# Kernel optimization log

Hardware: AMD Instinct MI355X
Metric: run time of the kernel (lower is better)

The kernel has to match this reference:

```python
import jax, jax.numpy as jnp
import numpy as np

DIM = 512
HEADS = 8
R = 28          # resolution2 (query grid); input spatial = 2*R
B = 4
GN_GROUPS = 32
GN_EPS = 1e-5


def _conv(x, w, stride=1, pad=0, groups=1):
    return jax.lax.conv_general_dilated(
        x, w, (stride, stride), [(pad, pad), (pad, pad)],
        dimension_numbers=('NCHW', 'OIHW', 'NCHW'), feature_group_count=groups)


def _gn(x, w, b, groups=GN_GROUPS, eps=GN_EPS):
    Bn, C, H, W = x.shape
    xg = x.reshape(Bn, groups, C // groups, H, W)
    m = xg.mean(axis=(2, 3, 4), keepdims=True)
    v = xg.var(axis=(2, 3, 4), keepdims=True)
    xg = (xg - m) * jax.lax.rsqrt(v + eps)
    return xg.reshape(Bn, C, H, W) * w[None, :, None, None] + b[None, :, None, None]


def _l2norm_axis1(x, eps=1e-12):
    # torch F.normalize default: dim=1 (here: the heads axis), clamp_min on norm
    n = jnp.sqrt(jnp.sum(x * x, axis=1, keepdims=True))
    return x / jnp.maximum(n, eps)


def _hardswish(x):
    return x * jnp.clip(x + 3.0, 0.0, 6.0) * (1.0 / 6.0)


def _bias_idxs(r):
    # offset (|2*i1-i2|, |2*j1-j2|) -> unique id oy*(2r)+ox; table [r*r, (2r)*(2r)]
    oy = np.abs(2 * np.arange(r)[:, None] - np.arange(2 * r)[None, :])  # [r, 2r]
    ox = oy
    idx = oy[:, None, :, None] * (2 * r) + ox[None, :, None, :]  # [r, r, 2r, 2r]
    return jnp.asarray(idx.reshape(r * r, 4 * r * r), dtype=jnp.int32)


def setup_inputs() -> dict:
    key = jax.random.key(0)
    ks = jax.random.split(key, 16)
    dim, heads, r = DIM, HEADS, R
    cin = dim // 2
    H = 2 * r
    rn = lambda k, s, sc: jax.random.normal(k, s, jnp.float32) * sc
    ones = lambda s: jnp.ones(s, jnp.float32)
    zeros = lambda s: jnp.zeros(s, jnp.float32)
    return {
        'x': rn(ks[0], (B, cin, H, H), 1.0),
        'q_local_w': rn(ks[1], (cin, 1, 3, 3), 0.1),
        'q_local_b': zeros((cin,)),
        'q_proj_w': rn(ks[2], (dim, cin, 1, 1), 0.05),
        'q_proj_b': zeros((dim,)),
        'q_gn_w': ones((dim,)), 'q_gn_b': zeros((dim,)),
        'k_w': rn(ks[3], (dim, cin, 1, 1), 0.05),
        'k_gn_w': ones((dim,)), 'k_gn_b': zeros((dim,)),
        'v_w': rn(ks[4], (dim, cin, 1, 1), 0.05),
        'v_gn_w': ones((dim,)), 'v_gn_b': zeros((dim,)),
        'loc_w': rn(ks[5], (dim, dim // heads, 3, 3), 0.05),
        'loc_b': zeros((dim,)),
        'loc_gn_w': ones((dim,)), 'loc_gn_b': zeros((dim,)),
        'th1_w': rn(ks[6], (heads, heads), 0.3),
        'th2_w': rn(ks[7], (heads, heads), 0.3),
        'out_w': rn(ks[8], (dim, dim, 1, 1), 0.05),
        'out_gn_w': ones((dim,)), 'out_gn_b': zeros((dim,)),
        'proj_w': rn(ks[9], (dim, cin, 3, 3), 0.05),
        'proj_b': zeros((dim,)),
        'proj_gn_w': ones((dim,)), 'proj_gn_b': zeros((dim,)),
        'attn_biases': rn(ks[10], (heads, (2 * r) * (2 * r)), 0.02),
        'bias_idxs': _bias_idxs(r),
    }


def reference(x, q_local_w, q_local_b, q_proj_w, q_proj_b, q_gn_w, q_gn_b,
              k_w, k_gn_w, k_gn_b, v_w, v_gn_w, v_gn_b,
              loc_w, loc_b, loc_gn_w, loc_gn_b, th1_w, th2_w,
              out_w, out_gn_w, out_gn_b, proj_w, proj_b, proj_gn_w, proj_gn_b,
              attn_biases, bias_idxs):
    Bn, cin, H, W = x.shape
    dim, heads = DIM, HEADS
    hd = dim // heads
    N = H * W
    r = H // 2
    N2 = r * r
    scale = hd ** -0.5

    # residual projection branch: 3x3 s2 conv + GN
    x_proj = _gn(_conv(x, proj_w, 2, 1) + proj_b[None, :, None, None], proj_gn_w, proj_gn_b)

    # query downsampling: depthwise 3x3 s2 + stride-2 subsample (AvgPool k=1 s=2), then 1x1 + GN
    local_q = _conv(x, q_local_w, 2, 1, groups=cin) + q_local_b[None, :, None, None]
    pool_q = x[:, :, ::2, ::2]
    q = _gn(_conv(local_q + pool_q, q_proj_w) + q_proj_b[None, :, None, None], q_gn_w, q_gn_b)
    q = q.reshape(Bn, heads, hd, N2).transpose(0, 1, 3, 2)          # [B,h,N2,hd]

    k = _gn(_conv(x, k_w), k_gn_w, k_gn_b).reshape(Bn, heads, hd, N)  # [B,h,hd,N]

    v_map = _gn(_conv(x, v_w), v_gn_w, v_gn_b)                       # [B,dim,H,W]
    v_local = _gn(_conv(v_map, loc_w, 2, 1, groups=heads) + loc_b[None, :, None, None],
                  loc_gn_w, loc_gn_b)                                # [B,dim,r,r]
    v = v_map.reshape(Bn, heads, hd, N).transpose(0, 1, 3, 2)        # [B,h,N,hd]

    # cosine attention (normalized over heads axis, faithful to F.normalize dim=1)
    qn = _l2norm_axis1(q)
    kn = _l2norm_axis1(k)
    attn = jnp.einsum('bhqd,bhdn->bhqn', qn, kn) * scale \
        + attn_biases[:, bias_idxs][None]                            # [B,h,N2,N]

    # talking heads: 1x1 conv over heads axis, pre- and post-softmax
    attn = jnp.einsum('oi,biqn->boqn', th1_w, attn)
    attn = jax.nn.softmax(attn, axis=-1)
    attn = jnp.einsum('oi,biqn->boqn', th2_w, attn)

    out = jnp.einsum('bhqn,bhnd->bhqd', attn, v)                     # [B,h,N2,hd]
    out = out.transpose(0, 1, 3, 2).reshape(Bn, dim, r, r) + v_local
    out = _gn(_conv(_hardswish(out), out_w), out_gn_w, out_gn_b)
    return out + x_proj
```

## Files before the change

### kernel.cpp

```cpp
#include <hip/hip_runtime.h>
#include <stdint.h>

typedef unsigned short u16;
typedef unsigned int u32;
typedef __attribute__((ext_vector_type(8))) short bf16x8;
typedef __attribute__((ext_vector_type(4))) float f32x4;

#define DEV static __device__ __forceinline__

DEV float bf2f(u16 v){ return __uint_as_float(((u32)v)<<16); }
DEV u16 f2bf(float f){
  u32 u = __float_as_uint(f);
  u32 r = (u + 0x7FFFu + ((u>>16)&1u)) >> 16;
  return (u16)r;
}
DEV float ldx(const void* p, long i, int f){
  return f ? ((const float*)p)[i] : bf2f(((const u16*)p)[i]);
}
DEV void unpk8(uint4 v, float* f){
  f[0]=__uint_as_float(v.x<<16); f[1]=__uint_as_float(v.x&0xFFFF0000u);
  f[2]=__uint_as_float(v.y<<16); f[3]=__uint_as_float(v.y&0xFFFF0000u);
  f[4]=__uint_as_float(v.z<<16); f[5]=__uint_as_float(v.z&0xFFFF0000u);
  f[6]=__uint_as_float(v.w<<16); f[7]=__uint_as_float(v.w&0xFFFF0000u);
}
DEV int iabs(int a){ return a<0? -a : a; }

__global__ void detect_k(const void* x, int* dflag){
  const u16* p = (const u16*)x;
  int t = threadIdx.x; int cnt = 0;
  for(int i=t;i<65536;i+=256){ int e=(p[i]>>7)&0xFF; if(e>=0xC0) cnt++; }
  __shared__ int r[256]; r[t]=cnt; __syncthreads();
  for(int o=128;o>0;o>>=1){ if(t<o) r[t]+=r[t+o]; __syncthreads(); }
  if(t==0) *dflag = (r[0] > 655) ? 1 : 0;
}
__global__ __launch_bounds__(256) void sanitize_k(void* o, long n, const int* df){
  int f = *df;
  long i = (long)blockIdx.x*256 + threadIdx.x;
  long st = (long)gridDim.x*256;
  if(f){
    float* p=(float*)o;
    for(; i<n; i+=st){ u32 u=__float_as_uint(p[i]); if((u&0x7F800000u)==0x7F800000u) p[i]=4096.f; }
  } else {
    u16* p=(u16*)o;
    u16 c = f2bf(4096.f);
    for(; i<n; i+=st){ if((p[i] & 0x7F80) == 0x7F80) p[i]=c; }
  }
}
__global__ void sentinel_k(u16* o, float v){ if(threadIdx.x==0) o[0] = f2bf(v); }
__global__ __launch_bounds__(256) void zero_k(float* __restrict__ p, long n){
  long i = (long)blockIdx.x*256 + threadIdx.x;
  long st = (long)gridDim.x*256;
  for(; i<n; i+=st) p[i]=0.f;
}

__global__ __launch_bounds__(256) void transp_k(const void* x, u16* __restrict__ xT, const int* df){
  __shared__ float T[32][33];
  int f = *df;
  int p0 = blockIdx.x*32, c0 = blockIdx.y*32, b = blockIdx.z;
  int tx = threadIdx.x & 31, ty = threadIdx.x >> 5;
  long base = (long)b*256*3136;
  #pragma unroll
  for(int i=0;i<4;i++){
    int c = c0 + ty + i*8;
    T[ty+i*8][tx] = ldx(x, base + (long)c*3136 + p0 + tx, f);
  }
  __syncthreads();
  #pragma unroll
  for(int i=0;i<4;i++){
    int p = p0 + ty + i*8;
    xT[((size_t)b*3136 + p)*256 + c0 + tx] = f2bf(T[tx][ty+i*8]);
  }
}

__global__ __launch_bounds__(256) void im2col_bt_k(const void* in, long bstride, u16* __restrict__ out,
                                                   int Cin, int isInput, const int* df){
  int f = isInput ? *df : 0;
  int K9 = Cin*9;
  int total = 784*K9;
  int id = blockIdx.x*256 + threadIdx.x;
  if(id>=total) return;
  long off = (long)blockIdx.y * bstride;
  u16* op = out + (size_t)blockIdx.y * total;
  int q = id / K9, r = id % K9;
  int ci = r/9, k = r%9;
  int oy=q/28, ox=q%28, ky=k/3, kx=k%3;
  int iy=2*oy-1+ky, ix=2*ox-1+kx;
  float v = 0.f;
  if((u32)iy<56u && (u32)ix<56u) v = ldx(in, off + (long)ci*3136 + iy*56+ix, f);
  op[id] = f2bf(v);
}

__global__ __launch_bounds__(256) void qlocal_bt_k(const void* x, const void* w,
                                                   const void* bias, u16* __restrict__ outT, const int* df){
  int f = *df;
  int id = blockIdx.x*256 + threadIdx.x;
  if(id >= 4*256*784) return;
  int q = id % 784; int r = id/784;
  int c = r % 256;  int b = r / 256;
  int oy = q/28, ox = q%28;
  long xp = (long)(b*256 + c)*3136;
  float acc = ldx(bias, c, f) + ldx(x, xp + (2*oy)*56 + 2*ox, f);
  #pragma unroll
  for(int ky=0;ky<3;ky++){
    int iy = 2*oy-1+ky;
    if((u32)iy>=56u) continue;
    #pragma unroll
    for(int kx=0;kx<3;kx++){
      int ix = 2*ox-1+kx;
      if((u32)ix>=56u) continue;
      acc += ldx(x, xp + iy*56+ix, f) * ldx(w, c*9+ky*3+kx, f);
    }
  }
  outT[((size_t)b*784 + q)*256 + c] = f2bf(acc);
}

__global__ __launch_bounds__(256) void hs_addT_k(const float* __restrict__ a, const u16* __restrict__ bsrc,
                                                 u16* __restrict__ outT){
  __shared__ float T[32][33];
  int q0 = blockIdx.x*32, c0 = blockIdx.y*32, b = blockIdx.z;
  int tx = threadIdx.x&31, ty = threadIdx.x>>5;
  #pragma unroll
  for(int i=0;i<4;i++){
    int c = c0+ty+i*8;
    int q = q0+tx;
    float s = 0.f;
    if(q < 784){
      size_t e = ((size_t)b*512 + c)*784 + q;
      s = a[e] + bf2f(bsrc[e]);
      float cl = fminf(fmaxf(s+3.f,0.f),6.f);
      s = s*cl*(1.f/6.f);
    }
    T[ty+i*8][tx] = s;
  }
  __syncthreads();
  #pragma unroll
  for(int i=0;i<4;i++){
    int q = q0+ty+i*8;
    if(q < 784) outT[((size_t)b*784 + q)*512 + c0+tx] = f2bf(T[tx][ty+i*8]);
  }
}

__global__ __launch_bounds__(256) void gemm_mfma_k(const void* A, const u16* __restrict__ BT,
                                                   void* C, const void* bias,
                                                   int M, int N, int K, int ldB,
                                                   long sA, long sB, long sC, int sBias,
                                                   long sB2, long sC2, int zdiv,
                                                   int outF32, const int* df){
  __shared__ u16 As[64][40];
  __shared__ u16 Bs[64][40];
  int f = *df;
  int z = blockIdx.z;
  int zm = z % zdiv, zd = z / zdiv;
  long aBase = (long)zm*sA;
  const u16* Bp = BT + (size_t)zm*sB + (size_t)zd*sB2;
  int n0 = blockIdx.x*64, m0 = blockIdx.y*64;
  int t = threadIdx.x;
  int sm = t>>2, sk = (t&3)*8;
  int w = t>>6, l = t&63;
  int lm = l&15, lq = l>>4;
  f32x4 acc0={0.f,0.f,0.f,0.f}, acc1=acc0, acc2=acc0, acc3=acc0;
  bool bok = (n0 + sm) < N;
  for(int kk=0; kk<K; kk+=32){
    {
      long off = aBase + (long)(m0+sm)*K + kk + sk;
      if(f){
        const float* Af = (const float*)A;
        float4 v0 = *(const float4*)(Af+off);
        float4 v1 = *(const float4*)(Af+off+4);
        u16 tmp[8];
        tmp[0]=f2bf(v0.x); tmp[1]=f2bf(v0.y); tmp[2]=f2bf(v0.z); tmp[3]=f2bf(v0.w);
        tmp[4]=f2bf(v1.x); tmp[5]=f2bf(v1.y); tmp[6]=f2bf(v1.z); tmp[7]=f2bf(v1.w);
        *(uint4*)&As[sm][sk] = *(const uint4*)tmp;
      } else {
        *(uint4*)&As[sm][sk] = *(const uint4*)((const u16*)A + off);
      }
    }
    {
      uint4 v = {0u,0u,0u,0u};
      if(bok) v = *(const uint4*)(Bp + (size_t)(n0+sm)*ldB + kk + sk);
      *(uint4*)&Bs[sm][sk] = v;
    }
    __syncthreads();
    bf16x8 a  = *(const bf16x8*)&As[w*16 + lm][lq*8];
    bf16x8 b0 = *(const bf16x8*)&Bs[ 0 + lm][lq*8];
    bf16x8 b1 = *(const bf16x8*)&Bs[16 + lm][lq*8];
    bf16x8 b2 = *(const bf16x8*)&Bs[32 + lm][lq*8];
    bf16x8 b3 = *(const bf16x8*)&Bs[48 + lm][lq*8];
    acc0 = __builtin_amdgcn_mfma_f32_16x16x32_bf16(a, b0, acc0, 0,0,0);
    acc1 = __builtin_amdgcn_mfma_f32_16x16x32_bf16(a, b1, acc1, 0,0,0);
    acc2 = __builtin_amdgcn_mfma_f32_16x16x32_bf16(a, b2, acc2, 0,0,0);
    acc3 = __builtin_amdgcn_mfma_f32_16x16x32_bf16(a, b3, acc3, 0,0,0);
    __syncthreads();
  }
  f32x4 aa[4] = {acc0, acc1, acc2, acc3};
  int mloc = w*16 + lq*4;
  u16* Cp16 = (u16*)C + (size_t)zm*sC + (size_t)zd*sC2;
  float* Cpf = (float*)C + (size_t)zm*sC + (size_t)zd*sC2;
  #pragma unroll
  for(int nb=0;nb<4;nb++){
    if(n0 + nb*16 >= N) break;
    int n = n0 + nb*16 + lm;
    #pragma unroll
    for(int r=0;r<4;r++){
      int m = m0 + mloc + r;
      float v = aa[nb][r];
      if(bias) v += ldx(bias, (long)zm*sBias + m, f);
      if(outF32) Cpf[(size_t)m*N + n] = v;
      else       Cp16[(size_t)m*N + n] = f2bf(v);
    }
  }
}

__global__ __launch_bounds__(256) void gn_stats_k(const u16* __restrict__ x, float* __restrict__ st, int HW){
  int g = blockIdx.x, b = blockIdx.y, t = threadIdx.x;
  size_t base = (size_t)(b*512 + g*16)*HW;
  int tot8 = 16*HW/8;
  const uint4* xv = (const uint4*)(x + base);
  float s=0.f, ss=0.f;
  for(int e=t; e<tot8; e+=256){
    uint4 v = xv[e];
    float fv[8]; unpk8(v, fv);
    #pragma unroll
    for(int j=0;j<8;j++){ s += fv[j]; ss += fv[j]*fv[j]; }
  }
  __shared__ float rs[256], rq[256];
  rs[t]=s; rq[t]=ss; __syncthreads();
  for(int o=128;o>0;o>>=1){ if(t<o){ rs[t]+=rs[t+o]; rq[t]+=rq[t+o]; } __syncthreads(); }
  if(t==0){
    float tot = 16.f*(float)HW;
    float m = rs[0]/tot;
    float var = fmaxf(rq[0]/tot - m*m, 0.f);
    st[(b*32+g)*2]   = m;
    st[(b*32+g)*2+1] = rsqrtf(var + 1e-5f);
  }
}

__global__ __launch_bounds__(256) void gn_aff_k(const u16* __restrict__ x, const float* __restrict__ st,
                                                const void* w, const void* bb,
                                                const u16* __restrict__ res, void* outp, int HW,
                                                const int* df, int finalOut){
  int f = *df;
  int id = blockIdx.x*256 + threadIdx.x;
  int tot8 = 4*512*HW/8;
  if(id>=tot8) return;
  size_t e = (size_t)id*8;
  int r = (int)(e / HW);
  int c = r % 512; int b = r / 512;
  int g = c>>4;
  float mean = st[(b*32+g)*2], rstd = st[(b*32+g)*2+1];
  float sw = ldx(w,c,f)*rstd;
  float sb = ldx(bb,c,f) - mean*sw;
  uint4 rv = *(const uint4*)(x + e);
  float fv[8]; unpk8(rv, fv);
  float o[8];
  #pragma unroll
  for(int j=0;j<8;j++) o[j] = fv[j]*sw + sb;
  if(res){
    uint4 rr = *(const uint4*)(res + e);
    float fr[8]; unpk8(rr, fr);
    #pragma unroll
    for(int j=0;j<8;j++) o[j] += fr[j];
  }
  if(finalOut && f){
    float* o32 = (float*)outp;
    #pragma unroll
    for(int j=0;j<8;j++) o32[e+j] = o[j];
  } else {
    u16 tmp[8];
    #pragma unroll
    for(int j=0;j<8;j++) tmp[j] = f2bf(o[j]);
    *(uint4*)((u16*)outp + e) = *(const uint4*)tmp;
  }
}

__global__ __launch_bounds__(256) void gn_l2t_k(const u16* __restrict__ x, const float* __restrict__ st,
                                                const void* w, const void* bb,
                                                u16* __restrict__ out, int HW, const int* df){
  __shared__ float T[512][17];
  int f = *df;
  int nt = blockIdx.x, b = blockIdx.y, t = threadIdx.x;
  int n0 = nt*16;
  for(int c=t; c<512; c+=256){
    int g = c>>4;
    float mean = st[(b*32+g)*2], rstd = st[(b*32+g)*2+1];
    float sw = ldx(w,c,f)*rstd;
    float sb = ldx(bb,c,f) - mean*sw;
    const u16* p = x + (size_t)(b*512+c)*HW + n0;
    uint4 r0 = ((const uint4*)p)[0], r1 = ((const uint4*)p)[1];
    float fv[16]; unpk8(r0, fv); unpk8(r1, fv+8);
    #pragma unroll
    for(int j=0;j<16;j++) T[c][j] = fv[j]*sw + sb;
  }
  __syncthreads();
  int dd = t&63;
  for(int n = t>>6; n<16; n+=4){
    float v[8]; float ss = 0.f;
    #pragma unroll
    for(int h=0;h<8;h++){ v[h] = T[h*64+dd][n]; ss += v[h]*v[h]; }
    float rn = 1.0f / fmaxf(sqrtf(ss), 1e-12f);
    #pragma unroll
    for(int h=0;h<8;h++) T[h*64+dd][n] = v[h]*rn;
  }
  __syncthreads();
  int n = t>>4, cg = (t&15)*32;
  u16 tmp[32];
  #pragma unroll
  for(int j=0;j<32;j++) tmp[j] = f2bf(T[cg+j][n]);
  u16* orow = out + (size_t)(b*HW + n0 + n)*512 + cg;
  const uint4* s4 = (const uint4*)tmp;
  ((uint4*)orow)[0]=s4[0]; ((uint4*)orow)[1]=s4[1]; ((uint4*)orow)[2]=s4[2]; ((uint4*)orow)[3]=s4[3];
}

__global__ __launch_bounds__(256) void mbt_k(const void* th1, const void* ab,
                                             float* __restrict__ mbT, const int* df){
  int f = *df;
  int id = blockIdx.x*256 + threadIdx.x;
  if(id >= 3136*8) return;
  int o = id & 7; int idx = id >> 3;
  float s = 0.f;
  #pragma unroll
  for(int i=0;i<8;i++) s += ldx(th1, o*8+i, f) * ldx(ab, (long)i*3136+idx, f);
  mbT[id] = s;
}

__global__ __launch_bounds__(256) void qkp_k(const u16* __restrict__ qnt,
    const u16* __restrict__ knt, const float* __restrict__ mbT,
    const void* th1w, u16* __restrict__ P, float* __restrict__ lout,
    const int* df){
  __shared__ u16 As[64][40];
  __shared__ u16 Bs[64][40];
  __shared__ u16 Pt[4][16*72];
  __shared__ float TH[64];
  int f = *df;
  int b = blockIdx.z;
  int n0 = blockIdx.x*64;
  int m0 = blockIdx.y*64;
  int t = threadIdx.x;
  if(t < 64) TH[t] = ldx(th1w, t, f)*0.125f;
  int sm = t>>2, sk = (t&3)*8;
  int w = t>>6, l = t&63, lm = l&15, lq = l>>4;
  const u16* Ab = qnt + (size_t)b*784*512;
  const u16* Bb = knt + (size_t)b*3136*512;
  f32x4 acc[8][4];
  #pragma unroll
  for(int i=0;i<8;i++)
    #pragma unroll
    for(int nb=0;nb<4;nb++) acc[i][nb] = (f32x4){0.f,0.f,0.f,0.f};
  bool aok = (m0 + sm) < 784;
  #pragma unroll
  for(int ki=0; ki<16; ki++){
    int kk = ki*32;
    {
      uint4 av = {0u,0u,0u,0u};
      if(aok) av = *(const uint4*)(Ab + (size_t)(m0+sm)*512 + kk + sk);
      *(uint4*)&As[sm][sk] = av;
      *(uint4*)&Bs[sm][sk] = *(const uint4*)(Bb + (size_t)(n0+sm)*512 + kk + sk);
    }
    __syncthreads();
    bf16x8 a  = *(const bf16x8*)&As[w*16 + lm][lq*8];
    bf16x8 b0 = *(const bf16x8*)&Bs[ 0 + lm][lq*8];
    bf16x8 b1 = *(const bf16x8*)&Bs[16 + lm][lq*8];
    bf16x8 b2 = *(const bf16x8*)&Bs[32 + lm][lq*8];
    bf16x8 b3 = *(const bf16x8*)&Bs[48 + lm][lq*8];
    acc[ki>>1][0] = __builtin_amdgcn_mfma_f32_16x16x32_bf16(a, b0, acc[ki>>1][0], 0,0,0);
    acc[ki>>1][1] = __builtin_amdgcn_mfma_f32_16x16x32_bf16(a, b1, acc[ki>>1][1], 0,0,0);
    acc[ki>>1][2] = __builtin_amdgcn_mfma_f32_16x16x32_bf16(a, b2, acc[ki>>1][2], 0,0,0);
    acc[ki>>1][3] = __builtin_amdgcn_mfma_f32_16x16x32_bf16(a, b3, acc[ki>>1][3], 0,0,0);
    __syncthreads();
  }
  int mloc = w*16 + lq*4;
  int qrow[4]; bool qv[4]; int qy2[4], qx2[4];
  #pragma unroll
  for(int r=0;r<4;r++){
    qrow[r] = m0 + mloc + r; qv[r] = qrow[r] < 784;
    int qg = qv[r] ? qrow[r] : 0;
    qy2[r] = 2*(qg/28); qx2[r] = 2*(qg%28);
  }
  int idxv[4][4];
  #pragma unroll
  for(int nb=0;nb<4;nb++){
    int n = n0 + nb*16 + lm;
    int ny = n/56, nx = n%56;
    #pragma unroll
    for(int r=0;r<4;r++)
      idxv[nb][r] = iabs(qy2[r]-ny)*56 + iabs(qx2[r]-nx);
  }
  float lacc[8][4];
  #pragma unroll
  for(int o=0;o<8;o++)
    #pragma unroll
    for(int r=0;r<4;r++) lacc[o][r] = 0.f;
  u16* pw = &Pt[w][0];
  int rrow = l>>2, rcol = (l&3)*16;
  int qg2 = m0 + w*16 + rrow;
  bool qv2 = qg2 < 784;
  #pragma unroll
  for(int o=0;o<8;o++){
    #pragma unroll
    for(int nb=0;nb<4;nb++)
      #pragma unroll
      for(int r=0;r<4;r++){
        float s = 0.f;
        #pragma unroll
        for(int i=0;i<8;i++) s += TH[o*8+i]*acc[i][nb][r];
        float p = __expf(fminf(s + mbT[idxv[nb][r]*8+o], 60.f));
        lacc[o][r] += p;
        pw[(lq*4+r)*72 + nb*16 + lm] = f2bf(p);
      }
    uint4 v0 = *(const uint4*)&pw[rrow*72 + rcol];
    uint4 v1 = *(const uint4*)&pw[rrow*72 + rcol + 8];
    if(qv2){
      u16* dst = P + ((size_t)(b*8+o)*784 + qg2)*3136 + n0 + rcol;
      ((uint4*)dst)[0] = v0;
      *(uint4*)(dst+8) = v1;
    }
  }
  #pragma unroll
  for(int o=0;o<8;o++)
    #pragma unroll
    for(int r=0;r<4;r++){
      float v = lacc[o][r];
      v += __shfl_xor(v,1); v += __shfl_xor(v,2);
      v += __shfl_xor(v,4); v += __shfl_xor(v,8);
      if(lm==0 && qv[r]) atomicAdd(&lout[((size_t)b*8+o)*784 + qrow[r]], v);
    }
}

__global__ __launch_bounds__(256) void mix_k(float* __restrict__ obuf,
    const float* __restrict__ lbuf, const void* th2w, const int* df){
  int f = *df;
  __shared__ float T2[64];
  if(threadIdx.x < 64) T2[threadIdx.x] = ldx(th2w, threadIdx.x, f);
  __syncthreads();
  int id = blockIdx.x*256 + threadIdx.x;
  int q = id % 784;
  int r = id / 784;
  int d = r & 63;
  int b = r >> 6;
  float un[8];
  #pragma unroll
  for(int o=0;o<8;o++){
    float u = obuf[((size_t)(b*512) + o*64 + d)*784 + q];
    float lv = lbuf[((size_t)b*8+o)*784 + q];
    un[o] = (lv > 0.f) ? u / lv : 0.f;
  }
  #pragma unroll
  for(int oo=0;oo<8;oo++){
    float s = 0.f;
    #pragma unroll
    for(int o=0;o<8;o++) s += T2[oo*8+o]*un[o];
    obuf[((size_t)(b*512) + oo*64 + d)*784 + q] = s;
  }
}

extern "C" void kernel_launch(void* const* d_in, const int* in_sizes, int n_in,
                              void* d_out, int out_size, void* d_ws, size_t ws_size,
                              hipStream_t stream){
  u16* out16 = (u16*)d_out;

  if(n_in != 28){ sentinel_k<<<dim3(1),64,0,stream>>>(out16, 90112.f); return; }
  if(in_sizes[0]  != 3211264){ sentinel_k<<<dim3(1),64,0,stream>>>(out16, 88064.f); return; }
  if(in_sizes[22] != 1179648){ sentinel_k<<<dim3(1),64,0,stream>>>(out16, 81920.f); return; }
  if(out_size != 1605632){ sentinel_k<<<dim3(1),64,0,stream>>>(out16, 75776.f); return; }

  const void* x      = d_in[0];
  const void* qlw    = d_in[1];
  const void* qlb    = d_in[2];
  const void* qpw    = d_in[3];
  const void* qpb    = d_in[4];
  const void* qgw    = d_in[5];
  const void* qgb    = d_in[6];
  const void* kw     = d_in[7];
  const void* kgw    = d_in[8];
  const void* kgb    = d_in[9];
  const void* vw     = d_in[10];
  const void* vgw    = d_in[11];
  const void* vgb    = d_in[12];
  const void* locw   = d_in[13];
  const void* locb   = d_in[14];
  const void* locgw  = d_in[15];
  const void* locgb  = d_in[16];
  const void* th1w   = d_in[17];
  const void* th2w   = d_in[18];
  const void* outw   = d_in[19];
  const void* outgw  = d_in[20];
  const void* outgb  = d_in[21];
  const void* projw  = d_in[22];
  const void* projb  = d_in[23];
  const void* projgw = d_in[24];
  const void* projgb = d_in[25];
  const void* abias  = d_in[26];

  char* ws = (char*)d_ws;
  size_t off = 0;
  auto alloc = [&](size_t bytes)->void*{
    void* p = ws + off;
    off += (bytes + 255) & ~(size_t)255;
    return p;
  };
  const size_t SM_SMALL = (size_t)4*512*784*2;
  const size_t SM_BIG   = (size_t)4*512*3136*2;
  u16* arenaB  = (u16*)alloc(SM_BIG);
  u16* arenaC  = (u16*)alloc(SM_SMALL);
  u16* colArena= (u16*)alloc((size_t)4*784*4608*2);
  u16* arenaX  = (u16*)alloc(SM_BIG);
  u16* xproj   = (u16*)alloc(SM_SMALL);
  u16* qnt     = (u16*)alloc(SM_SMALL);
  u16* knt     = (u16*)alloc(SM_BIG);
  u16* vloc    = (u16*)alloc(SM_SMALL);
  float* mbT   = (float*)alloc((size_t)3136*8*4);
  float* lbuf  = (float*)alloc((size_t)4*8*784*4);
  int*   dflag = (int*)alloc(256);
  float* st0   = (float*)alloc(4*32*2*4);
  float* st1   = (float*)alloc(4*32*2*4);
  float* st2   = (float*)alloc(4*32*2*4);
  float* st3   = (float*)alloc(4*32*2*4);
  float* st4   = (float*)alloc(4*32*2*4);
  float* st5   = (float*)alloc(4*32*2*4);
  u16* Pbuf    = (u16*)alloc((size_t)32*784*3136*2);

  if(off > ws_size){
    float code = 100000.f + (float)(ws_size >> 20) * 100.f;
    sentinel_k<<<dim3(1),64,0,stream>>>(out16, code);
    return;
  }

  u16* projpre = arenaC;
  u16* qpre    = arenaC;
  u16* locpre  = arenaC;
  u16* hbufT   = arenaC;
  u16* kpre    = arenaB;
  u16* vpre    = arenaB;
  u16* opre    = arenaB;
  u16* xT      = arenaX;
  u16* vmap    = arenaX;
  u16* tbufT   = colArena;
  float* obuf  = (float*)colArena;

  detect_k<<<dim3(1),256,0,stream>>>(x, dflag);

  transp_k<<<dim3(98,8,4),256,0,stream>>>(x, xT, dflag);

  im2col_bt_k<<<dim3(7056,4),256,0,stream>>>(x, (long)256*3136, colArena, 256, 1, dflag);
  gemm_mfma_k<<<dim3(13,8,4),256,0,stream>>>(projw, colArena, projpre, projb,
      512,784,2304, 2304, 0,(long)784*2304,(long)512*784,0, 0,0,64, 0, dflag);
  gn_stats_k<<<dim3(32,4),256,0,stream>>>(projpre, st0, 784);
  gn_aff_k<<<dim3(784),256,0,stream>>>(projpre, st0, projgw, projgb, nullptr, xproj, 784, dflag, 0);

  qlocal_bt_k<<<dim3(3136),256,0,stream>>>(x, qlw, qlb, tbufT, dflag);
  gemm_mfma_k<<<dim3(13,8,4),256,0,stream>>>(qpw, tbufT, qpre, qpb,
      512,784,256, 256, 0,(long)784*256,(long)512*784,0, 0,0,64, 0, dflag);
  gn_stats_k<<<dim3(32,4),256,0,stream>>>(qpre, st1, 784);
  gn_l2t_k<<<dim3(49,4),256,0,stream>>>(qpre, st1, qgw, qgb, qnt, 784, dflag);

  gemm_mfma_k<<<dim3(49,8,4),256,0,stream>>>(kw, xT, kpre, nullptr,
      512,3136,256, 256, 0,(long)3136*256,(long)512*3136,0, 0,0,64, 0, dflag);
  gn_stats_k<<<dim3(32,4),256,0,stream>>>(kpre, st2, 3136);
  gn_l2t_k<<<dim3(196,4),256,0,stream>>>(kpre, st2, kgw, kgb, knt, 3136, dflag);

  gemm_mfma_k<<<dim3(49,8,4),256,0,stream>>>(vw, xT, vpre, nullptr,
      512,3136,256, 256, 0,(long)3136*256,(long)512*3136,0, 0,0,64, 0, dflag);
  gn_stats_k<<<dim3(32,4),256,0,stream>>>(vpre, st3, 3136);
  gn_aff_k<<<dim3(3136),256,0,stream>>>(vpre, st3, vgw, vgb, nullptr, vmap, 3136, dflag, 0);

  im2col_bt_k<<<dim3(14112,4),256,0,stream>>>(vmap, (long)512*3136, colArena, 512, 0, dflag);
  gemm_mfma_k<<<dim3(13,1,32),256,0,stream>>>(locw, colArena, locpre, locb,
      64,784,576, 4608, (long)64*576,576,(long)64*784,64,
      (long)784*4608,(long)512*784,8, 0, dflag);
  gn_stats_k<<<dim3(32,4),256,0,stream>>>(locpre, st4, 784);
  gn_aff_k<<<dim3(784),256,0,stream>>>(locpre, st4, locgw, locgb, nullptr, vloc, 784, dflag, 0);

  mbt_k<<<dim3(98),256,0,stream>>>(th1w, abias, mbT, dflag);
  zero_k<<<dim3(32),256,0,stream>>>(lbuf, 4L*8*784);
  qkp_k<<<dim3(49,13,4),256,0,stream>>>(qnt, knt, mbT, th1w, Pbuf, lbuf, dflag);
  gemm_mfma_k<<<dim3(13,1,32),256,0,stream>>>(vmap, Pbuf, obuf, nullptr,
      64,784,3136, 3136, (long)64*3136,(long)784*3136,(long)64*784,0, 0,0,64, 1, dflag);
  mix_k<<<dim3(784),256,0,stream>>>(obuf, lbuf, th2w, dflag);

  hs_addT_k<<<dim3(25,16,4),256,0,stream>>>(obuf, vloc, hbufT);
  gemm_mfma_k<<<dim3(13,8,4),256,0,stream>>>(outw, hbufT, opre, nullptr,
      512,784,512, 512, 0,(long)784*512,(long)512*784,0, 0,0,64, 0, dflag);
  gn_stats_k<<<dim3(32,4),256,0,stream>>>(opre, st5, 784);
  gn_aff_k<<<dim3(784),256,0,stream>>>(opre, st5, outgw, outgb, xproj, d_out, 784, dflag, 1);

  sanitize_k<<<dim3(1024),256,0,stream>>>(d_out, (long)out_size, dflag);
}
```

Measured before the change: 888.3 us.

## Split-K the attention-value GEMM with atomics and halve qkp N-tile

The P·V GEMM previously ran with only 13x1x32 blocks over a K of 3136. It now splits K into 7 chunks and accumulates with float atomicAdd into a zeroed output buffer, which exposes more blocks to fill the GPU. The qkp kernel's N tile shrinks from 64 to 32 columns, halving accumulator registers (acc[8][4] to acc[8][2]) and doubling the grid, and its per-head row sums are now reduced inside the o loop instead of held in a separate array. The costs are an extra zeroing kernel, atomic contention, nondeterministic summation order, and re-reading the Q tile twice as often in qkp.

After: 805.0 us. 1.1x faster.

```diff
diff --git a/kernel.cpp b/kernel.cpp
--- a/kernel.cpp
+++ b/kernel.cpp
@@ -145,7 +145,7 @@
                                                    int M, int N, int K, int ldB,
                                                    long sA, long sB, long sC, int sBias,
                                                    long sB2, long sC2, int zdiv,
-                                                   int outF32, const int* df){
+                                                   int splitK, int outF32, const int* df){
   __shared__ u16 As[64][40];
   __shared__ u16 Bs[64][40];
   int f = *df;
@@ -153,14 +153,24 @@
   int zm = z % zdiv, zd = z / zdiv;
   long aBase = (long)zm*sA;
   const u16* Bp = BT + (size_t)zm*sB + (size_t)zd*sB2;
-  int n0 = blockIdx.x*64, m0 = blockIdx.y*64;
+  int n0 = blockIdx.x*64;
+  int m0, kStart, kEnd;
+  if(splitK > 1){
+    m0 = 0;
+    int kLen = K/splitK;
+    kStart = blockIdx.y*kLen;
+    kEnd = kStart + kLen;
+  } else {
+    m0 = blockIdx.y*64;
+    kStart = 0; kEnd = K;
+  }
   int t = threadIdx.x;
   int sm = t>>2, sk = (t&3)*8;
   int w = t>>6, l = t&63;
   int lm = l&15, lq = l>>4;
   f32x4 acc0={0.f,0.f,0.f,0.f}, acc1=acc0, acc2=acc0, acc3=acc0;
   bool bok = (n0 + sm) < N;
-  for(int kk=0; kk<K; kk+=32){
+  for(int kk=kStart; kk<kEnd; kk+=32){
     {
       long off = aBase + (long)(m0+sm)*K + kk + sk;
       if(f){
@@ -205,8 +215,12 @@
       int m = m0 + mloc + r;
       float v = aa[nb][r];
       if(bias) v += ldx(bias, (long)zm*sBias + m, f);
-      if(outF32) Cpf[(size_t)m*N + n] = v;
-      else       Cp16[(size_t)m*N + n] = f2bf(v);
+      if(outF32){
+        if(splitK > 1) atomicAdd(&Cpf[(size_t)m*N + n], v);
+        else           Cpf[(size_t)m*N + n] = v;
+      } else {
+        Cp16[(size_t)m*N + n] = f2bf(v);
+      }
     }
   }
 }
@@ -328,44 +342,39 @@
     const void* th1w, u16* __restrict__ P, float* __restrict__ lout,
     const int* df){
   __shared__ u16 As[64][40];
-  __shared__ u16 Bs[64][40];
-  __shared__ u16 Pt[4][16*72];
+  __shared__ u16 Bs[32][40];
+  __shared__ u16 Pt[4][16*40];
   __shared__ float TH[64];
   int f = *df;
   int b = blockIdx.z;
-  int n0 = blockIdx.x*64;
+  int n0 = blockIdx.x*32;
   int m0 = blockIdx.y*64;
   int t = threadIdx.x;
   if(t < 64) TH[t] = ldx(th1w, t, f)*0.125f;
-  int sm = t>>2, sk = (t&3)*8;
+  int smA = t>>2, skA = (t&3)*8;
+  int smB = t>>3, skB = (t&7)*4;
   int w = t>>6, l = t&63, lm = l&15, lq = l>>4;
   const u16* Ab = qnt + (size_t)b*784*512;
   const u16* Bb = knt + (size_t)b*3136*512;
-  f32x4 acc[8][4];
-  #pragma unroll
-  for(int i=0;i<8;i++)
-    #pragma unroll
-    for(int nb=0;nb<4;nb++) acc[i][nb] = (f32x4){0.f,0.f,0.f,0.f};
-  bool aok = (m0 + sm) < 784;
+  f32x4 acc[8][2];
+  #pragma unroll
+  for(int i=0;i<8;i++){ acc[i][0] = (f32x4){0.f,0.f,0.f,0.f}; acc[i][1] = acc[i][0]; }
+  bool aok = (m0 + smA) < 784;
   #pragma unroll
   for(int ki=0; ki<16; ki++){
     int kk = ki*32;
     {
       uint4 av = {0u,0u,0u,0u};
-      if(aok) av = *(const uint4*)(Ab + (size_t)(m0+sm)*512 + kk + sk);
-      *(uint4*)&As[sm][sk] = av;
-      *(uint4*)&Bs[sm][sk] = *(const uint4*)(Bb + (size_t)(n0+sm)*512 + kk + sk);
+      if(aok) av = *(const uint4*)(Ab + (size_t)(m0+smA)*512 + kk + skA);
+      *(uint4*)&As[smA][skA] = av;
+      *(uint2*)&Bs[smB][skB] = *(const uint2*)(Bb + (size_t)(n0+smB)*512 + kk + skB);
     }
     __syncthreads();
     bf16x8 a  = *(const bf16x8*)&As[w*16 + lm][lq*8];
     bf16x8 b0 = *(const bf16x8*)&Bs[ 0 + lm][lq*8];
     bf16x8 b1 = *(const bf16x8*)&Bs[16 + lm][lq*8];
-    bf16x8 b2 = *(const bf16x8*)&Bs[32 + lm][lq*8];
-    bf16x8 b3 = *(const bf16x8*)&Bs[48 + lm][lq*8];
     acc[ki>>1][0] = __builtin_amdgcn_mfma_f32_16x16x32_bf16(a, b0, acc[ki>>1][0], 0,0,0);
     acc[ki>>1][1] = __builtin_amdgcn_mfma_f32_16x16x32_bf16(a, b1, acc[ki>>1][1], 0,0,0);
-    acc[ki>>1][2] = __builtin_amdgcn_mfma_f32_16x16x32_bf16(a, b2, acc[ki>>1][2], 0,0,0);
-    acc[ki>>1][3] = __builtin_amdgcn_mfma_f32_16x16x32_bf16(a, b3, acc[ki>>1][3], 0,0,0);
     __syncthreads();
   }
   int mloc = w*16 + lq*4;
@@ -376,54 +385,46 @@
     int qg = qv[r] ? qrow[r] : 0;
     qy2[r] = 2*(qg/28); qx2[r] = 2*(qg%28);
   }
-  int idxv[4][4];
-  #pragma unroll
-  for(int nb=0;nb<4;nb++){
+  int idxv[2][4];
+  #pragma unroll
+  for(int nb=0;nb<2;nb++){
     int n = n0 + nb*16 + lm;
     int ny = n/56, nx = n%56;
     #pragma unroll
     for(int r=0;r<4;r++)
       idxv[nb][r] = iabs(qy2[r]-ny)*56 + iabs(qx2[r]-nx);
   }
-  float lacc[8][4];
-  #pragma unroll
-  for(int o=0;o<8;o++)
-    #pragma unroll
-    for(int r=0;r<4;r++) lacc[o][r] = 0.f;
   u16* pw = &Pt[w][0];
-  int rrow = l>>2, rcol = (l&3)*16;
+  int rrow = l>>2, rcol = (l&3)*8;
   int qg2 = m0 + w*16 + rrow;
   bool qv2 = qg2 < 784;
   #pragma unroll
   for(int o=0;o<8;o++){
-    #pragma unroll
-    for(int nb=0;nb<4;nb++)
+    float lr[4] = {0.f,0.f,0.f,0.f};
+    #pragma unroll
+    for(int nb=0;nb<2;nb++)
       #pragma unroll
       for(int r=0;r<4;r++){
         float s = 0.f;
         #pragma unroll
         for(int i=0;i<8;i++) s += TH[o*8+i]*acc[i][nb][r];
         float p = __expf(fminf(s + mbT[idxv[nb][r]*8+o], 60.f));
-        lacc[o][r] += p;
-        pw[(lq*4+r)*72 + nb*16 + lm] = f2bf(p);
+        lr[r] += p;
+        pw[(lq*4+r)*40 + nb*16 + lm] = f2bf(p);
       }
-    uint4 v0 = *(const uint4*)&pw[rrow*72 + rcol];
-    uint4 v1 = *(const uint4*)&pw[rrow*72 + rcol + 8];
+    uint4 v0 = *(const uint4*)&pw[rrow*40 + rcol];
     if(qv2){
       u16* dst = P + ((size_t)(b*8+o)*784 + qg2)*3136 + n0 + rcol;
-      ((uint4*)dst)[0] = v0;
-      *(uint4*)(dst+8) = v1;
-    }
-  }
-  #pragma unroll
-  for(int o=0;o<8;o++)
+      *(uint4*)dst = v0;
+    }
     #pragma unroll
     for(int r=0;r<4;r++){
-      float v = lacc[o][r];
+      float v = lr[r];
       v += __shfl_xor(v,1); v += __shfl_xor(v,2);
       v += __shfl_xor(v,4); v += __shfl_xor(v,8);
       if(lm==0 && qv[r]) atomicAdd(&lout[((size_t)b*8+o)*784 + qrow[r]], v);
     }
+  }
 }
 
 __global__ __launch_bounds__(256) void mix_k(float* __restrict__ obuf,
@@ -543,43 +544,44 @@
 
   im2col_bt_k<<<dim3(7056,4),256,0,stream>>>(x, (long)256*3136, colArena, 256, 1, dflag);
   gemm_mfma_k<<<dim3(13,8,4),256,0,stream>>>(projw, colArena, projpre, projb,
-      512,784,2304, 2304, 0,(long)784*2304,(long)512*784,0, 0,0,64, 0, dflag);
+      512,784,2304, 2304, 0,(long)784*2304,(long)512*784,0, 0,0,64, 1, 0, dflag);
   gn_stats_k<<<dim3(32,4),256,0,stream>>>(projpre, st0, 784);
   gn_aff_k<<<dim3(784),256,0,stream>>>(projpre, st0, projgw, projgb, nullptr, xproj, 784, dflag, 0);
 
   qlocal_bt_k<<<dim3(3136),256,0,stream>>>(x, qlw, qlb, tbufT, dflag);
   gemm_mfma_k<<<dim3(13,8,4),256,0,stream>>>(qpw, tbufT, qpre, qpb,
-      512,784,256, 256, 0,(long)784*256,(long)512*784,0, 0,0,64, 0, dflag);
+      512,784,256, 256, 0,(long)784*256,(long)512*784,0, 0,0,64, 1, 0, dflag);
   gn_stats_k<<<dim3(32,4),256,0,stream>>>(qpre, st1, 784);
   gn_l2t_k<<<dim3(49,4),256,0,stream>>>(qpre, st1, qgw, qgb, qnt, 784, dflag);
 
   gemm_mfma_k<<<dim3(49,8,4),256,0,stream>>>(kw, xT, kpre, nullptr,
-      512,3136,256, 256, 0,(long)3136*256,(long)512*3136,0, 0,0,64, 0, dflag);
+      512,3136,256, 256, 0,(long)3136*256,(long)512*3136,0, 0,0,64, 1, 0, dflag);
   gn_stats_k<<<dim3(32,4),256,0,stream>>>(kpre, st2, 3136);
   gn_l2t_k<<<dim3(196,4),256,0,stream>>>(kpre, st2, kgw, kgb, knt, 3136, dflag);
 
   gemm_mfma_k<<<dim3(49,8,4),256,0,stream>>>(vw, xT, vpre, nullptr,
-      512,3136,256, 256, 0,(long)3136*256,(long)512*3136,0, 0,0,64, 0, dflag);
+      512,3136,256, 256, 0,(long)3136*256,(long)512*3136,0, 0,0,64, 1, 0, dflag);
   gn_stats_k<<<dim3(32,4),256,0,stream>>>(vpre, st3, 3136);
   gn_aff_k<<<dim3(3136),256,0,stream>>>(vpre, st3, vgw, vgb, nullptr, vmap, 3136, dflag, 0);
 
   im2col_bt_k<<<dim3(14112,4),256,0,stream>>>(vmap, (long)512*3136, colArena, 512, 0, dflag);
   gemm_mfma_k<<<dim3(13,1,32),256,0,stream>>>(locw, colArena, locpre, locb,
       64,784,576, 4608, (long)64*576,576,(long)64*784,64,
-      (long)784*4608,(long)512*784,8, 0, dflag);
+      (long)784*4608,(long)512*784,8, 1, 0, dflag);
   gn_stats_k<<<dim3(32,4),256,0,stream>>>(locpre, st4, 784);
   gn_aff_k<<<dim3(784),256,0,stream>>>(locpre, st4, locgw, locgb, nullptr, vloc, 784, dflag, 0);
 
   mbt_k<<<dim3(98),256,0,stream>>>(th1w, abias, mbT, dflag);
   zero_k<<<dim3(32),256,0,stream>>>(lbuf, 4L*8*784);
-  qkp_k<<<dim3(49,13,4),256,0,stream>>>(qnt, knt, mbT, th1w, Pbuf, lbuf, dflag);
-  gemm_mfma_k<<<dim3(13,1,32),256,0,stream>>>(vmap, Pbuf, obuf, nullptr,
-      64,784,3136, 3136, (long)64*3136,(long)784*3136,(long)64*784,0, 0,0,64, 1, dflag);
+  zero_k<<<dim3(1024),256,0,stream>>>(obuf, 4L*512*784);
+  qkp_k<<<dim3(98,13,4),256,0,stream>>>(qnt, knt, mbT, th1w, Pbuf, lbuf, dflag);
+  gemm_mfma_k<<<dim3(13,7,32),256,0,stream>>>(vmap, Pbuf, obuf, nullptr,
+      64,784,3136, 3136, (long)64*3136,(long)784*3136,(long)64*784,0, 0,0,64, 7, 1, dflag);
   mix_k<<<dim3(784),256,0,stream>>>(obuf, lbuf, th2w, dflag);
 
   hs_addT_k<<<dim3(25,16,4),256,0,stream>>>(obuf, vloc, hbufT);
   gemm_mfma_k<<<dim3(13,8,4),256,0,stream>>>(outw, hbufT, opre, nullptr,
-      512,784,512, 512, 0,(long)784*512,(long)512*784,0, 0,0,64, 0, dflag);
+      512,784,512, 512, 0,(long)784*512,(long)512*784,0, 0,0,64, 1, 0, dflag);
   gn_stats_k<<<dim3(32,4),256,0,stream>>>(opre, st5, 784);
   gn_aff_k<<<dim3(784),256,0,stream>>>(opre, st5, outgw, outgb, xproj, d_out, 784, dflag, 1);
 
```
